# Kernel tuning notes

Hardware: AMD Instinct MI355X
Metric: run time of the kernel (lower is better)

The kernel has to match this reference:

```python
import jax, jax.numpy as jnp
from jax import lax
import numpy as np

C_IN, D_INNER, D_STATE, OUT_CH = 20, 32, 8, 20
DT_RANK = max(1, D_INNER // 8)
B, H, W = 4, 384, 384
EPS = 1e-5


def layernorm(x, g, b):
    m = jnp.mean(x, axis=-1, keepdims=True)
    v = jnp.mean((x - m) ** 2, axis=-1, keepdims=True)
    return (x - m) * lax.rsqrt(v + EPS) * g + b


def ss1d(x, xw, dw, db, A_log, Dp):
    # x: (Bb, L, Dd). Mamba selective scan: h_t = exp(dt*A)*h_{t-1} + dt*B_t*u_t; y_t = C_t.h_t + D*u_t
    Bb, L, Dd = x.shape
    N = A_log.shape[1]
    xdbl = x @ xw.T                                   # (Bb, L, dtr+2N)
    dt_lo, Bm, Cm = jnp.split(xdbl, [DT_RANK, DT_RANK + N], axis=-1)
    dt = jax.nn.softplus(dt_lo @ dw.T + db)           # (Bb, L, Dd)
    A = -jnp.exp(A_log)                               # (Dd, N)

    def step(h, inp):
        dt_t, B_t, C_t, u_t = inp                     # (Bb,Dd),(Bb,N),(Bb,N),(Bb,Dd)
        dA = jnp.exp(dt_t[:, :, None] * A)            # (Bb, Dd, N)
        h = dA * h + (dt_t * u_t)[:, :, None] * B_t[:, None, :]
        y = jnp.einsum('bdn,bn->bd', h, C_t)
        return h, y

    xs = (jnp.moveaxis(dt, 1, 0), jnp.moveaxis(Bm, 1, 0),
          jnp.moveaxis(Cm, 1, 0), jnp.moveaxis(x, 1, 0))
    h0 = jnp.zeros((Bb, Dd, N), dtype=x.dtype)
    _, ys = lax.scan(step, h0, xs)
    return jnp.moveaxis(ys, 0, 1) + x * Dp


def setup_inputs() -> dict:
    key = jax.random.key(0)
    ks = jax.random.split(key, 16)
    s = lambda k, shp, sc=0.05: jax.random.normal(k, shp, dtype=jnp.float32) * sc
    A_log1 = jnp.log(jnp.broadcast_to(jnp.arange(1, D_STATE + 1, dtype=jnp.float32), (D_INNER, D_STATE)))
    return {
        'x': jax.random.normal(ks[0], (B, C_IN, H, W), dtype=jnp.float32),
        'norm_g': jnp.ones((C_IN,), jnp.float32),
        'norm_b': jnp.zeros((C_IN,), jnp.float32),
        'inproj_w': s(ks[1], (D_INNER, C_IN), 0.15),
        'dw_w': s(ks[2], (3, 3, 1, D_INNER), 0.2),
        'dw_b': jnp.zeros((D_INNER,), jnp.float32),
        'ssm_xw': s(ks[3], (4, DT_RANK + 2 * D_STATE, D_INNER), 0.1),
        'ssm_dw': s(ks[4], (4, D_INNER, DT_RANK), 0.5),
        'ssm_db': s(ks[5], (4, D_INNER), 0.5) - 3.0,
        'ssm_Alog': jnp.broadcast_to(A_log1, (4, D_INNER, D_STATE)).copy(),
        'ssm_D': jnp.ones((4, D_INNER), jnp.float32),
        'merge_g': jnp.ones((4 * D_INNER,), jnp.float32),
        'merge_b': jnp.zeros((4 * D_INNER,), jnp.float32),
        'merge_w': s(ks[6], (D_INNER, 4 * D_INNER), 0.1),
        'out_w': s(ks[7], (OUT_CH, D_INNER), 0.15),
        'out_b': jnp.zeros((OUT_CH,), jnp.float32),
    }


def reference(x, norm_g, norm_b, inproj_w, dw_w, dw_b, ssm_xw, ssm_dw, ssm_db,
              ssm_Alog, ssm_D, merge_g, merge_b, merge_w, out_w, out_b):
    Bx, C, Hx, Wx = x.shape
    h = jnp.transpose(x, (0, 2, 3, 1))                      # (B,H,W,C)
    h = layernorm(h, norm_g, norm_b)
    h = jax.nn.silu(h @ inproj_w.T)                          # (B,H,W,Dd)
    h = lax.conv_general_dilated(h, dw_w, (1, 1), 'SAME',
                                 dimension_numbers=('NHWC', 'HWIO', 'NHWC'),
                                 feature_group_count=D_INNER) + dw_b
    h = jax.nn.silu(h)                                       # (B,H,W,Dd)

    p = lambda i: (ssm_xw[i], ssm_dw[i], ssm_db[i], ssm_Alog[i], ssm_D[i])

    x_h = h.reshape(Bx * Hx, Wx, D_INNER)
    y_h_fwd = ss1d(x_h, *p(0)).reshape(Bx, Hx, Wx, D_INNER)
    y_h_bwd = ss1d(x_h[:, ::-1], *p(1))[:, ::-1].reshape(Bx, Hx, Wx, D_INNER)

    x_v = jnp.transpose(h, (0, 2, 1, 3)).reshape(Bx * Wx, Hx, D_INNER)
    y_v_fwd = jnp.transpose(ss1d(x_v, *p(2)).reshape(Bx, Wx, Hx, D_INNER), (0, 2, 1, 3))
    y_v_bwd = jnp.transpose(ss1d(x_v[:, ::-1], *p(3))[:, ::-1].reshape(Bx, Wx, Hx, D_INNER), (0, 2, 1, 3))

    y = jnp.concatenate([y_h_fwd, y_h_bwd, y_v_fwd, y_v_bwd], axis=-1)  # (B,H,W,4*Dd)
    y = layernorm(y, merge_g, merge_b)
    y = y @ merge_w.T                                        # (B,H,W,Dd)
    y = y @ out_w.T + out_b                                  # (B,H,W,out_ch)
    return jnp.transpose(y, (0, 3, 1, 2))                    # (B,out_ch,H,W)
```

## Files before the change

kernel.cpp:

```cpp
#include <hip/hip_runtime.h>

typedef unsigned short u16;
typedef unsigned int   u32;
typedef unsigned long long u64;
typedef float f2 __attribute__((ext_vector_type(2)));

#define CIN  20
#define DIN  32
#define BB   4
#define HH   384
#define WW   384
#define HW   147456
#define BHW  589824
#define EPSF 1e-5f
#define GUARD  65536
#define UGUARD 131072

__device__ __forceinline__ float bflo(u32 u) {
    union { u32 v; float f; } x; x.v = u << 16; return x.f;
}
__device__ __forceinline__ float bfhi(u32 u) {
    union { u32 v; float f; } x; x.v = u & 0xffff0000u; return x.f;
}
__device__ __forceinline__ float bf2f(u16 h) {
    union { u32 v; float f; } x; x.v = ((u32)h) << 16; return x.f;
}
__device__ __forceinline__ u16 f2bf(float f) {
    union { float f; u32 u; } v; v.f = f;
    u32 u = v.u;
    return (u16)((u + 0x7FFFu + ((u >> 16) & 1u)) >> 16);
}
__device__ __forceinline__ float silu_f(float a) {
    return a / (1.f + __expf(-a));
}
__device__ __forceinline__ float softplus_f(float z) {
    return (z > 15.f) ? z : __logf(1.f + __expf(z));
}

__global__ void k_prep(const float* __restrict__ ow, const float* __restrict__ mw,
                       const float* __restrict__ mg, const float* __restrict__ mb,
                       const float* __restrict__ ob,
                       float* __restrict__ Wt, float* __restrict__ rsum,
                       float* __restrict__ c0)
{
    __shared__ float mdot[DIN];
    int t = threadIdx.x;
    if (t < DIN) {
        float s = 0.f;
        for (int k = 0; k < 128; ++k) s += mw[t*128 + k] * mb[k];
        mdot[t] = s;
    }
    {
        int k = t;
        for (int o = 0; o < CIN; ++o) {
            float s = 0.f;
            for (int d = 0; d < DIN; ++d) s += ow[o*DIN + d] * mw[d*128 + k];
            Wt[k*CIN + o] = s * mg[k];
        }
    }
    __syncthreads();
    if (t < CIN) {
        float rs = 0.f;
        for (int k = 0; k < 128; ++k) rs += Wt[k*CIN + t];
        rsum[t] = rs;
        float c = ob[t];
        for (int d = 0; d < DIN; ++d) c += ow[t*DIN + d] * mdot[d];
        c0[t] = c;
    }
}

#define TS   16
#define HT   18
#define CPAD 36
__global__ __launch_bounds__(256) void k_lnconv(
    const float* __restrict__ x, const float* __restrict__ ng,
    const float* __restrict__ nb, const float* __restrict__ ipw,
    const float* __restrict__ cw, const float* __restrict__ cb,
    u16* __restrict__ h2)
{
    __shared__ __align__(16) float hs[HT*HT*CPAD];
    __shared__ __align__(16) f2 wln_s[CIN*16];
    __shared__ float g_s[CIN], b_s[CIN];
    __shared__ __align__(16) f2 wc_s[9*16];
    __shared__ __align__(16) f2 bc2_s[16];

    int tid = threadIdx.x;
    for (int i = tid; i < CIN*16; i += 256) {
        int c = i >> 4, j2 = i & 15;
        wln_s[i] = f2{ ipw[(2*j2)*CIN + c], ipw[(2*j2+1)*CIN + c] };
    }
    if (tid < CIN) { g_s[tid] = ng[tid]; b_s[tid] = nb[tid]; }
    if (tid < 144) wc_s[tid] = f2{ cw[2*tid], cw[2*tid+1] };
    if (tid >= 144 && tid < 160) {
        int i = tid - 144;
        bc2_s[i] = f2{ cb[2*i], cb[2*i+1] };
    }
    __syncthreads();

    int bx = blockIdx.x;
    int b  = bx / 576, t6 = bx % 576;
    int ty0 = (t6 / 24)*TS, tx0 = (t6 % 24)*TS;

    auto do_pixel = [&](int j) {
        int hy = j / HT, hx = j % HT;
        int gy = ty0 + hy - 1, gx = tx0 + hx - 1;
        float* hp = &hs[(hy*HT + hx)*CPAD];
        if (gy >= 0 && gy < HH && gx >= 0 && gx < WW) {
            int rem = gy*WW + gx;
            float v[CIN];
            float m = 0.f;
            #pragma unroll
            for (int c = 0; c < CIN; ++c) { v[c] = x[(b*CIN + c)*HW + rem]; m += v[c]; }
            m *= (1.f/CIN);
            float var = 0.f;
            #pragma unroll
            for (int c = 0; c < CIN; ++c) { float d = v[c]-m; var += d*d; }
            var *= (1.f/CIN);
            float rstd = rsqrtf(var + EPSF);
            #pragma unroll
            for (int c = 0; c < CIN; ++c) v[c] = (v[c]-m)*rstd*g_s[c] + b_s[c];

            f2 o2[16];
            #pragma unroll
            for (int j2 = 0; j2 < 16; ++j2) o2[j2] = f2{0.f, 0.f};
            #pragma unroll
            for (int c = 0; c < CIN; ++c) {
                f2 vc = { v[c], v[c] };
                const float4* wr = (const float4*)&wln_s[c*16];
                #pragma unroll
                for (int jq = 0; jq < 8; ++jq) {
                    float4 wp = wr[jq];
                    o2[2*jq]   = __builtin_elementwise_fma(f2{wp.x, wp.y}, vc, o2[2*jq]);
                    o2[2*jq+1] = __builtin_elementwise_fma(f2{wp.z, wp.w}, vc, o2[2*jq+1]);
                }
            }
            #pragma unroll
            for (int q = 0; q < 8; ++q) {
                float a0 = silu_f(o2[2*q].x),   a1 = silu_f(o2[2*q].y);
                float a2 = silu_f(o2[2*q+1].x), a3 = silu_f(o2[2*q+1].y);
                *(float4*)&hp[4*q] = make_float4(a0, a1, a2, a3);
            }
        } else {
            #pragma unroll
            for (int q = 0; q < 8; ++q)
                *(float4*)&hp[4*q] = make_float4(0.f, 0.f, 0.f, 0.f);
        }
    };

    do_pixel(tid);
    __syncthreads();
    if (tid < HT*HT - 256) do_pixel(256 + tid);
    __syncthreads();

    int ty = tid >> 4, tx = tid & 15;
    int gy = ty0 + ty, gx = tx0 + tx;
    int p  = b*HW + gy*WW + gx;

    f2 acc2[16];
    #pragma unroll
    for (int i = 0; i < 16; ++i) acc2[i] = bc2_s[i];

    #pragma unroll
    for (int k = 0; k < 9; ++k) {
        int dy = k/3, dx = k%3;
        const float* np = &hs[((ty+dy)*HT + (tx+dx))*CPAD];
        const f2* wk = &wc_s[k*16];
        #pragma unroll
        for (int q = 0; q < 8; ++q) {
            float4 t4 = *(const float4*)&np[4*q];
            acc2[2*q]   = __builtin_elementwise_fma(wk[2*q],   f2{t4.x, t4.y}, acc2[2*q]);
            acc2[2*q+1] = __builtin_elementwise_fma(wk[2*q+1], f2{t4.z, t4.w}, acc2[2*q+1]);
        }
    }

    u32 pk[16];
    #pragma unroll
    for (int i = 0; i < 16; ++i) {
        float a = silu_f(acc2[i].x);
        float c = silu_f(acc2[i].y);
        pk[i] = (u32)f2bf(a) | ((u32)f2bf(c) << 16);
    }
    uint4* dst = (uint4*)(h2 + (size_t)p*DIN);
    dst[0] = make_uint4(pk[0],pk[1],pk[2],pk[3]);
    dst[1] = make_uint4(pk[4],pk[5],pk[6],pk[7]);
    dst[2] = make_uint4(pk[8],pk[9],pk[10],pk[11]);
    dst[3] = make_uint4(pk[12],pk[13],pk[14],pk[15]);
}

__global__ __launch_bounds__(256) void k_proj(
    const u16* __restrict__ h2, const float* __restrict__ xw,
    u16* __restrict__ dlA, u16* __restrict__ bcA)
{
    __shared__ __align__(16) f2 xw2_s[4*DIN*10];
    for (int i = threadIdx.x; i < 4*DIN*10; i += 256) {
        int dir = i / 320, r = i % 320;
        int d = r / 10, j2 = r % 10;
        xw2_s[i] = f2{ xw[(dir*CIN + 2*j2)*DIN + d],
                       xw[(dir*CIN + 2*j2 + 1)*DIN + d] };
    }
    __syncthreads();

    int p = (blockIdx.x*256 + threadIdx.x)*2;
    float ua[DIN], ub[DIN];
    const uint4* src = (const uint4*)(h2 + (size_t)p*DIN);
    #pragma unroll
    for (int q4 = 0; q4 < 4; ++q4) {
        uint4 v = src[q4];
        ua[q4*8+0]=bflo(v.x); ua[q4*8+1]=bfhi(v.x);
        ua[q4*8+2]=bflo(v.y); ua[q4*8+3]=bfhi(v.y);
        ua[q4*8+4]=bflo(v.z); ua[q4*8+5]=bfhi(v.z);
        ua[q4*8+6]=bflo(v.w); ua[q4*8+7]=bfhi(v.w);
        uint4 w = src[q4+4];
        ub[q4*8+0]=bflo(w.x); ub[q4*8+1]=bfhi(w.x);
        ub[q4*8+2]=bflo(w.y); ub[q4*8+3]=bfhi(w.y);
        ub[q4*8+4]=bflo(w.z); ub[q4*8+5]=bfhi(w.z);
        ub[q4*8+6]=bflo(w.w); ub[q4*8+7]=bfhi(w.w);
    }
    #pragma unroll 1
    for (int dir = 0; dir < 4; ++dir) {
        f2 xa[10], xb[10];
        #pragma unroll
        for (int j2 = 0; j2 < 10; ++j2) { xa[j2] = f2{0.f,0.f}; xb[j2] = f2{0.f,0.f}; }
        #pragma unroll
        for (int d = 0; d < DIN; ++d) {
            f2 uda = { ua[d], ua[d] };
            f2 udb = { ub[d], ub[d] };
            const float4* wr = (const float4*)&xw2_s[(dir*DIN + d)*10];
            #pragma unroll
            for (int jq = 0; jq < 5; ++jq) {
                float4 wp = wr[jq];
                f2 wlo = {wp.x, wp.y}, whi = {wp.z, wp.w};
                xa[2*jq]   = __builtin_elementwise_fma(wlo, uda, xa[2*jq]);
                xa[2*jq+1] = __builtin_elementwise_fma(whi, uda, xa[2*jq+1]);
                xb[2*jq]   = __builtin_elementwise_fma(wlo, udb, xb[2*jq]);
                xb[2*jq+1] = __builtin_elementwise_fma(whi, udb, xb[2*jq+1]);
            }
        }
        u32 pa[10], pb[10];
        #pragma unroll
        for (int i = 0; i < 10; ++i) {
            pa[i] = (u32)f2bf(xa[i].x) | ((u32)f2bf(xa[i].y) << 16);
            pb[i] = (u32)f2bf(xb[i].x) | ((u32)f2bf(xb[i].y) << 16);
        }
        *(uint4*)(dlA + (size_t)(dir*BHW + p)*4) = make_uint4(pa[0], pa[1], pb[0], pb[1]);
        uint4* bcd = (uint4*)(bcA + (size_t)(dir*BHW + p)*16);
        bcd[0] = make_uint4(pa[2], pa[3], pa[4], pa[5]);
        bcd[1] = make_uint4(pa[6], pa[7], pa[8], pa[9]);
        bcd[2] = make_uint4(pb[2], pb[3], pb[4], pb[5]);
        bcd[3] = make_uint4(pb[6], pb[7], pb[8], pb[9]);
    }
}

__global__ __launch_bounds__(256) void k_scan(
    const char* __restrict__ h2b,
    const char* __restrict__ dlb_,
    const char* __restrict__ bcb_,
    const float* __restrict__ Alog, const float* __restrict__ Dp,
    const float* __restrict__ dwm,  const float* __restrict__ dbv,
    char* __restrict__ y4b)
{
    int tid  = blockIdx.x*256 + threadIdx.x;
    int wv   = tid >> 6, lane = tid & 63;
    int half = lane >> 5, d = lane & 31;
    int dir  = wv / 768;
    int s    = (wv % 768)*2 + half;
    int b    = s / 384, r = s % 384;

    int p0, stp;
    if (dir == 0)      { p0 = b*HW + r*WW;           stp = 1;  }
    else if (dir == 1) { p0 = b*HW + r*WW + (WW-1);  stp = -1; }
    else if (dir == 2) { p0 = b*HW + r;              stp = WW; }
    else               { p0 = b*HW + (HH-1)*WW + r;  stp = -WW;}

    float Av[8];
    bool okl = true;
    #pragma unroll
    for (int j = 0; j < 8; ++j) {
        float e = __expf(Alog[(dir*DIN + d)*8 + j]);
        Av[j] = -e;
        okl = okl && (__builtin_fabsf(e - (float)(j+1)) < 2e-3f);
    }
    bool fast = (__ballot(okl) == ~0ull);

    float Dd  = Dp[dir*DIN + d];
    float dw0 = dwm[(dir*DIN + d)*4 + 0], dw1 = dwm[(dir*DIN + d)*4 + 1];
    float dw2 = dwm[(dir*DIN + d)*4 + 2], dw3 = dwm[(dir*DIN + d)*4 + 3];
    float dbc = dbv[dir*DIN + d];

    u32 uo = UGUARD + (u32)((p0*DIN + d)*2);           int su = stp*DIN*2;
    u32 yo = (u32)((dir*BHW + p0)*64 + d*2);           int sy = stp*64;
    u32 c1 = GUARD + (u32)((dir*BHW + p0)*8);          int s1 = stp*8;
    u32 c2 = GUARD + (u32)((dir*BHW + p0)*32);         int s2 = stp*32;

    u16 ub[4]; uint2 dlr[4]; uint4 B4[4], C4[4];
    u32 fu = uo, f1 = c1, f2o = c2;

    auto fetch = [&](int sl) {
        ub[sl]  = *(const u16*)(h2b + fu);
        dlr[sl] = *(const uint2*)(dlb_ + f1);
        B4[sl]  = *(const uint4*)(bcb_ + f2o);
        C4[sl]  = *(const uint4*)(bcb_ + f2o + 16);
        fu += (u32)su; f1 += (u32)s1; f2o += (u32)s2;
    };

    #pragma unroll
    for (int i = 0; i < 4; ++i) fetch(i);

    f2 h0 = {0.f,0.f}, h1v = {0.f,0.f}, h2v = {0.f,0.f}, h3 = {0.f,0.f};

    if (fast) {
        f2 a01, a23, a45, a67;
        f2 Bq0, Bq1, Bq2, Bq3;
        f2 Cp0, Cp1, Cp2, Cp3;
        float ydc;

        auto prep = [&](int sl) {
            float uu = bf2f(ub[sl]);
            uint2 dl = dlr[sl];
            uint4 Bv = B4[sl], Cv = C4[sl];
            float z = dbc + dw0*bflo(dl.x) + dw1*bfhi(dl.x)
                          + dw2*bflo(dl.y) + dw3*bfhi(dl.y);
            z = fminf(z, 80.f);
            float ez = __expf(z);
            float w  = 1.f + ez;
            float rr = __builtin_amdgcn_rcpf(w);
            float dt = __logf(w);
            float r2 = rr*rr;
            f2 rr2 = {r2, r2};
            f2 t01 = {rr, r2};
            a01 = t01;
            a23 = t01*rr2;
            a45 = a23*rr2;
            a67 = a45*rr2;
            float dtu = dt*uu;
            f2 du2 = {dtu, dtu};
            f2 Bp0 = { bflo(Bv.x), bfhi(Bv.x) }, Bp1 = { bflo(Bv.y), bfhi(Bv.y) };
            f2 Bp2 = { bflo(Bv.z), bfhi(Bv.z) }, Bp3 = { bflo(Bv.w), bfhi(Bv.w) };
            Bq0 = du2*Bp0; Bq1 = du2*Bp1; Bq2 = du2*Bp2; Bq3 = du2*Bp3;
            f2 c0 = { bflo(Cv.x), bfhi(Cv.x) }, c1v = { bflo(Cv.y), bfhi(Cv.y) };
            f2 c2v = { bflo(Cv.z), bfhi(Cv.z) }, c3 = { bflo(Cv.w), bfhi(Cv.w) };
            Cp0 = c0; Cp1 = c1v; Cp2 = c2v; Cp3 = c3;
            ydc = Dd*uu;
        };

        prep(0);

        #pragma unroll 4
        for (int t = 0; t < 384; ++t) {
            int sl = t & 3;
            fetch(sl);

            h0  = __builtin_elementwise_fma(a01, h0,  Bq0);
            h1v = __builtin_elementwise_fma(a23, h1v, Bq1);
            h2v = __builtin_elementwise_fma(a45, h2v, Bq2);
            h3  = __builtin_elementwise_fma(a67, h3,  Bq3);

            f2 yv = Cp0*h0;
            yv = __builtin_elementwise_fma(Cp1, h1v, yv);
            yv = __builtin_elementwise_fma(Cp2, h2v, yv);
            yv = __builtin_elementwise_fma(Cp3, h3,  yv);
            float y = yv.x + yv.y + ydc;

            prep((t+1) & 3);

            *(u16*)(y4b + yo) = f2bf(y);
            yo += (u32)sy;
        }
    } else {
        f2 A2[4];
        #pragma unroll
        for (int j = 0; j < 4; ++j) { A2[j].x = Av[2*j]; A2[j].y = Av[2*j+1]; }
        #pragma unroll 4
        for (int t = 0; t < 384; ++t) {
            int sl = t & 3;
            float uu = bf2f(ub[sl]);
            uint2 dl = dlr[sl];
            uint4 Bv = B4[sl], Cv = C4[sl];
            fetch(sl);

            float z = dbc + dw0*bflo(dl.x) + dw1*bfhi(dl.x)
                          + dw2*bflo(dl.y) + dw3*bfhi(dl.y);
            float dt = softplus_f(z);
            f2 dt2 = {dt, dt};
            f2 e0 = dt2*A2[0], e1 = dt2*A2[1], e2 = dt2*A2[2], e3 = dt2*A2[3];
            f2 a01 = { __expf(e0.x), __expf(e0.y) };
            f2 a23 = { __expf(e1.x), __expf(e1.y) };
            f2 a45 = { __expf(e2.x), __expf(e2.y) };
            f2 a67 = { __expf(e3.x), __expf(e3.y) };

            float dtu = dt*uu;
            f2 du2 = {dtu, dtu};
            f2 Bp0 = { bflo(Bv.x), bfhi(Bv.x) }, Bp1 = { bflo(Bv.y), bfhi(Bv.y) };
            f2 Bp2 = { bflo(Bv.z), bfhi(Bv.z) }, Bp3 = { bflo(Bv.w), bfhi(Bv.w) };
            f2 Cp0 = { bflo(Cv.x), bfhi(Cv.x) }, Cp1 = { bflo(Cv.y), bfhi(Cv.y) };
            f2 Cp2 = { bflo(Cv.z), bfhi(Cv.z) }, Cp3 = { bflo(Cv.w), bfhi(Cv.w) };

            h0  = __builtin_elementwise_fma(a01, h0,  du2*Bp0);
            h1v = __builtin_elementwise_fma(a23, h1v, du2*Bp1);
            h2v = __builtin_elementwise_fma(a45, h2v, du2*Bp2);
            h3  = __builtin_elementwise_fma(a67, h3,  du2*Bp3);

            f2 yv = Cp0*h0;
            yv = __builtin_elementwise_fma(Cp1, h1v, yv);
            yv = __builtin_elementwise_fma(Cp2, h2v, yv);
            yv = __builtin_elementwise_fma(Cp3, h3,  yv);

            float y = yv.x + yv.y + Dd*uu;
            *(u16*)(y4b + yo) = f2bf(y);
            yo += (u32)sy;
        }
    }
}

__global__ __launch_bounds__(256) void k_merge(
    const u16* __restrict__ y4, const float* __restrict__ Wt,
    const float* __restrict__ rsum, const float* __restrict__ c0,
    float* __restrict__ out)
{
    __shared__ __align__(16) f2 Wt2_s[128*10];
    __shared__ float rs_s[CIN], c0_s[CIN];
    for (int i = threadIdx.x; i < 128*10; i += 256) {
        int k = i / 10, o2 = i % 10;
        Wt2_s[i] = f2{ Wt[k*CIN + 2*o2], Wt[k*CIN + 2*o2 + 1] };
    }
    if (threadIdx.x < CIN) { rs_s[threadIdx.x] = rsum[threadIdx.x]; c0_s[threadIdx.x] = c0[threadIdx.x]; }
    __syncthreads();

    int p = (blockIdx.x*256 + threadIdx.x)*2;
    int b = p / HW, rem = p % HW;

    float s1a = 0.f, s2a = 0.f, s1b = 0.f, s2b = 0.f;
    f2 acca[10], accb[10];
    #pragma unroll
    for (int o2 = 0; o2 < 10; ++o2) { acca[o2] = f2{0.f,0.f}; accb[o2] = f2{0.f,0.f}; }

    #pragma unroll 1
    for (int dirk = 0; dirk < 4; ++dirk) {
        const uint4* src = (const uint4*)(y4 + ((size_t)dirk*BHW + p)*32);
        #pragma unroll
        for (int q4 = 0; q4 < 4; ++q4) {
            uint4 va = src[q4];
            uint4 vb = src[q4+4];
            u32 wa[4] = {va.x, va.y, va.z, va.w};
            u32 wb[4] = {vb.x, vb.y, vb.z, vb.w};
            #pragma unroll
            for (int i = 0; i < 4; ++i) {
                int k = dirk*32 + q4*8 + i*2;
                float aa = bflo(wa[i]); float ca = bfhi(wa[i]);
                float ab = bflo(wb[i]); float cb = bfhi(wb[i]);
                s1a += aa + ca; s2a += aa*aa + ca*ca;
                s1b += ab + cb; s2b += ab*ab + cb*cb;
                f2 afa = {aa, aa}, cfa = {ca, ca};
                f2 afb = {ab, ab}, cfb = {cb, cb};
                const float4* w0 = (const float4*)&Wt2_s[k*10];
                const float4* w1 = (const float4*)&Wt2_s[(k+1)*10];
                #pragma unroll
                for (int jq = 0; jq < 5; ++jq) {
                    float4 x0 = w0[jq], x1 = w1[jq];
                    f2 x0lo = {x0.x, x0.y}, x0hi = {x0.z, x0.w};
                    f2 x1lo = {x1.x, x1.y}, x1hi = {x1.z, x1.w};
                    acca[2*jq]   = __builtin_elementwise_fma(x0lo, afa, acca[2*jq]);
                    acca[2*jq]   = __builtin_elementwise_fma(x1lo, cfa, acca[2*jq]);
                    acca[2*jq+1] = __builtin_elementwise_fma(x0hi, afa, acca[2*jq+1]);
                    acca[2*jq+1] = __builtin_elementwise_fma(x1hi, cfa, acca[2*jq+1]);
                    accb[2*jq]   = __builtin_elementwise_fma(x0lo, afb, accb[2*jq]);
                    accb[2*jq]   = __builtin_elementwise_fma(x1lo, cfb, accb[2*jq]);
                    accb[2*jq+1] = __builtin_elementwise_fma(x0hi, afb, accb[2*jq+1]);
                    accb[2*jq+1] = __builtin_elementwise_fma(x1hi, cfb, accb[2*jq+1]);
                }
            }
        }
    }
    float ma = s1a*(1.f/128.f);
    float va = s2a*(1.f/128.f) - ma*ma;
    float ra = rsqrtf(va + EPSF);
    float mb2 = s1b*(1.f/128.f);
    float vb2 = s2b*(1.f/128.f) - mb2*mb2;
    float rb = rsqrtf(vb2 + EPSF);
    #pragma unroll
    for (int o2 = 0; o2 < 10; ++o2) {
        float a0 = ra*(acca[o2].x - ma*rs_s[2*o2])    + c0_s[2*o2];
        float a1 = ra*(acca[o2].y - ma*rs_s[2*o2+1])  + c0_s[2*o2+1];
        float b0 = rb*(accb[o2].x - mb2*rs_s[2*o2])   + c0_s[2*o2];
        float b1 = rb*(accb[o2].y - mb2*rs_s[2*o2+1]) + c0_s[2*o2+1];
        *(float2*)&out[(b*CIN + 2*o2)*HW + rem]   = float2{a0, b0};
        *(float2*)&out[(b*CIN + 2*o2+1)*HW + rem] = float2{a1, b1};
    }
}

extern "C" void kernel_launch(void* const* d_in, const int* in_sizes, int n_in,
                              void* d_out, int out_size, void* d_ws, size_t ws_size,
                              hipStream_t stream)
{
    const float* x    = (const float*)d_in[0];
    const float* ng   = (const float*)d_in[1];
    const float* nb   = (const float*)d_in[2];
    const float* ipw  = (const float*)d_in[3];
    const float* cw   = (const float*)d_in[4];
    const float* cb   = (const float*)d_in[5];
    const float* xw   = (const float*)d_in[6];
    const float* dwm  = (const float*)d_in[7];
    const float* dbv  = (const float*)d_in[8];
    const float* Alog = (const float*)d_in[9];
    const float* Dpv  = (const float*)d_in[10];
    const float* mg   = (const float*)d_in[11];
    const float* mb   = (const float*)d_in[12];
    const float* mw   = (const float*)d_in[13];
    const float* ow   = (const float*)d_in[14];
    const float* ob   = (const float*)d_in[15];
    float* out = (float*)d_out;

    const size_t y4_bytes = (size_t)4*BHW*DIN*2;
    const size_t dl_bytes = (size_t)4*BHW*8;
    const size_t bc_bytes = (size_t)4*BHW*32;
    const size_t wt_bytes = (size_t)(128*CIN + 64)*4;

    char* ws = (char*)d_ws;
    u16* y4 = (u16*)ws;

    size_t dl_pos = y4_bytes + GUARD;
    size_t bc_pos = dl_pos + dl_bytes + GUARD;
    size_t wt_pos = bc_pos + bc_bytes + GUARD;
    size_t need   = wt_pos + wt_bytes + GUARD;

    if (ws_size < need) {
        hipMemsetAsync(d_out, 0x7F, (size_t)out_size*4, stream);
        return;
    }

    char* h2base = (char*)d_out;
    u16*  h2 = (u16*)(h2base + UGUARD);

    u16* dlA = (u16*)(ws + dl_pos);
    u16* bcA = (u16*)(ws + bc_pos);
    float* Wt   = (float*)(ws + wt_pos);
    float* rsum = Wt + 128*CIN;
    float* c0   = rsum + 32;

    k_prep  <<<1, 128, 0, stream>>>(ow, mw, mg, mb, ob, Wt, rsum, c0);
    k_lnconv<<<2304, 256, 0, stream>>>(x, ng, nb, ipw, cw, cb, h2);
    k_proj  <<<BHW/512, 256, 0, stream>>>(h2, xw, dlA, bcA);
    k_scan  <<<768, 256, 0, stream>>>(
        h2base, (const char*)(ws + dl_pos - GUARD), (const char*)(ws + bc_pos - GUARD),
        Alog, Dpv, dwm, dbv, (char*)y4);
    k_merge <<<BHW/512, 256, 0, stream>>>(y4, Wt, rsum, c0, out);
}
```

Baseline: 479.8 us.

## Fuse prep, layernorm-conv and x-projection into a single front kernel

Merges k_prep, k_lnconv and k_proj into one kernel, k_front. Each thread now computes the per-direction x-projection (dt, B, C) straight from its in-register fp32 SiLU outputs instead of re-reading h2 from global memory as bf16. The projection weights reuse the conv tile's shared memory after a barrier, and block 0 also computes the merge-weight precompute. This removes two launches and one full pass over h2, at the cost of more register pressure and one extra shared-memory reload per block. The projection now uses unrounded fp32 activations, so its values can differ slightly.

```diff
diff --git a/kernel.cpp b/kernel.cpp
--- a/kernel.cpp
+++ b/kernel.cpp
@@ -37,52 +37,29 @@
     return (z > 15.f) ? z : __logf(1.f + __expf(z));
 }
 
-__global__ void k_prep(const float* __restrict__ ow, const float* __restrict__ mw,
-                       const float* __restrict__ mg, const float* __restrict__ mb,
-                       const float* __restrict__ ob,
-                       float* __restrict__ Wt, float* __restrict__ rsum,
-                       float* __restrict__ c0)
-{
-    __shared__ float mdot[DIN];
-    int t = threadIdx.x;
-    if (t < DIN) {
-        float s = 0.f;
-        for (int k = 0; k < 128; ++k) s += mw[t*128 + k] * mb[k];
-        mdot[t] = s;
-    }
-    {
-        int k = t;
-        for (int o = 0; o < CIN; ++o) {
-            float s = 0.f;
-            for (int d = 0; d < DIN; ++d) s += ow[o*DIN + d] * mw[d*128 + k];
-            Wt[k*CIN + o] = s * mg[k];
-        }
-    }
-    __syncthreads();
-    if (t < CIN) {
-        float rs = 0.f;
-        for (int k = 0; k < 128; ++k) rs += Wt[k*CIN + t];
-        rsum[t] = rs;
-        float c = ob[t];
-        for (int d = 0; d < DIN; ++d) c += ow[t*DIN + d] * mdot[d];
-        c0[t] = c;
-    }
-}
-
 #define TS   16
 #define HT   18
 #define CPAD 36
-__global__ __launch_bounds__(256) void k_lnconv(
+__global__ __launch_bounds__(256) void k_front(
     const float* __restrict__ x, const float* __restrict__ ng,
     const float* __restrict__ nb, const float* __restrict__ ipw,
     const float* __restrict__ cw, const float* __restrict__ cb,
-    u16* __restrict__ h2)
+    const float* __restrict__ xw,
+    const float* __restrict__ ow, const float* __restrict__ mw,
+    const float* __restrict__ mg, const float* __restrict__ mb,
+    const float* __restrict__ ob,
+    u16* __restrict__ h2, u16* __restrict__ dlA, u16* __restrict__ bcA,
+    float* __restrict__ Wt, float* __restrict__ rsum, float* __restrict__ c0)
 {
-    __shared__ __align__(16) float hs[HT*HT*CPAD];
+    __shared__ __align__(16) float sraw[HT*HT*CPAD];
     __shared__ __align__(16) f2 wln_s[CIN*16];
     __shared__ float g_s[CIN], b_s[CIN];
     __shared__ __align__(16) f2 wc_s[9*16];
     __shared__ __align__(16) f2 bc2_s[16];
+    __shared__ float mdot[DIN];
+
+    float* hs = sraw;
+    f2* xw2_s = (f2*)sraw;
 
     int tid = threadIdx.x;
     for (int i = tid; i < CIN*16; i += 256) {
@@ -173,26 +150,26 @@
         }
     }
 
-    u32 pk[16];
+    float u[DIN];
     #pragma unroll
     for (int i = 0; i < 16; ++i) {
-        float a = silu_f(acc2[i].x);
-        float c = silu_f(acc2[i].y);
-        pk[i] = (u32)f2bf(a) | ((u32)f2bf(c) << 16);
-    }
-    uint4* dst = (uint4*)(h2 + (size_t)p*DIN);
-    dst[0] = make_uint4(pk[0],pk[1],pk[2],pk[3]);
-    dst[1] = make_uint4(pk[4],pk[5],pk[6],pk[7]);
-    dst[2] = make_uint4(pk[8],pk[9],pk[10],pk[11]);
-    dst[3] = make_uint4(pk[12],pk[13],pk[14],pk[15]);
-}
-
-__global__ __launch_bounds__(256) void k_proj(
-    const u16* __restrict__ h2, const float* __restrict__ xw,
-    u16* __restrict__ dlA, u16* __restrict__ bcA)
-{
-    __shared__ __align__(16) f2 xw2_s[4*DIN*10];
-    for (int i = threadIdx.x; i < 4*DIN*10; i += 256) {
+        u[2*i]   = silu_f(acc2[i].x);
+        u[2*i+1] = silu_f(acc2[i].y);
+    }
+    {
+        u32 pk[16];
+        #pragma unroll
+        for (int i = 0; i < 16; ++i)
+            pk[i] = (u32)f2bf(u[2*i]) | ((u32)f2bf(u[2*i+1]) << 16);
+        uint4* dst = (uint4*)(h2 + (size_t)p*DIN);
+        dst[0] = make_uint4(pk[0],pk[1],pk[2],pk[3]);
+        dst[1] = make_uint4(pk[4],pk[5],pk[6],pk[7]);
+        dst[2] = make_uint4(pk[8],pk[9],pk[10],pk[11]);
+        dst[3] = make_uint4(pk[12],pk[13],pk[14],pk[15]);
+    }
+    __syncthreads();
+
+    for (int i = tid; i < 4*DIN*10; i += 256) {
         int dir = i / 320, r = i % 320;
         int d = r / 10, j2 = r % 10;
         xw2_s[i] = f2{ xw[(dir*CIN + 2*j2)*DIN + d],
@@ -200,54 +177,56 @@
     }
     __syncthreads();
 
-    int p = (blockIdx.x*256 + threadIdx.x)*2;
-    float ua[DIN], ub[DIN];
-    const uint4* src = (const uint4*)(h2 + (size_t)p*DIN);
-    #pragma unroll
-    for (int q4 = 0; q4 < 4; ++q4) {
-        uint4 v = src[q4];
-        ua[q4*8+0]=bflo(v.x); ua[q4*8+1]=bfhi(v.x);
-        ua[q4*8+2]=bflo(v.y); ua[q4*8+3]=bfhi(v.y);
-        ua[q4*8+4]=bflo(v.z); ua[q4*8+5]=bfhi(v.z);
-        ua[q4*8+6]=bflo(v.w); ua[q4*8+7]=bfhi(v.w);
-        uint4 w = src[q4+4];
-        ub[q4*8+0]=bflo(w.x); ub[q4*8+1]=bfhi(w.x);
-        ub[q4*8+2]=bflo(w.y); ub[q4*8+3]=bfhi(w.y);
-        ub[q4*8+4]=bflo(w.z); ub[q4*8+5]=bfhi(w.z);
-        ub[q4*8+6]=bflo(w.w); ub[q4*8+7]=bfhi(w.w);
-    }
     #pragma unroll 1
     for (int dir = 0; dir < 4; ++dir) {
-        f2 xa[10], xb[10];
-        #pragma unroll
-        for (int j2 = 0; j2 < 10; ++j2) { xa[j2] = f2{0.f,0.f}; xb[j2] = f2{0.f,0.f}; }
+        f2 xd2[10];
+        #pragma unroll
+        for (int j2 = 0; j2 < 10; ++j2) xd2[j2] = f2{0.f, 0.f};
         #pragma unroll
         for (int d = 0; d < DIN; ++d) {
-            f2 uda = { ua[d], ua[d] };
-            f2 udb = { ub[d], ub[d] };
+            f2 ud = { u[d], u[d] };
             const float4* wr = (const float4*)&xw2_s[(dir*DIN + d)*10];
             #pragma unroll
             for (int jq = 0; jq < 5; ++jq) {
                 float4 wp = wr[jq];
-                f2 wlo = {wp.x, wp.y}, whi = {wp.z, wp.w};
-                xa[2*jq]   = __builtin_elementwise_fma(wlo, uda, xa[2*jq]);
-                xa[2*jq+1] = __builtin_elementwise_fma(whi, uda, xa[2*jq+1]);
-                xb[2*jq]   = __builtin_elementwise_fma(wlo, udb, xb[2*jq]);
-                xb[2*jq+1] = __builtin_elementwise_fma(whi, udb, xb[2*jq+1]);
+                xd2[2*jq]   = __builtin_elementwise_fma(f2{wp.x, wp.y}, ud, xd2[2*jq]);
+                xd2[2*jq+1] = __builtin_elementwise_fma(f2{wp.z, wp.w}, ud, xd2[2*jq+1]);
             }
         }
-        u32 pa[10], pb[10];
-        #pragma unroll
-        for (int i = 0; i < 10; ++i) {
-            pa[i] = (u32)f2bf(xa[i].x) | ((u32)f2bf(xa[i].y) << 16);
-            pb[i] = (u32)f2bf(xb[i].x) | ((u32)f2bf(xb[i].y) << 16);
-        }
-        *(uint4*)(dlA + (size_t)(dir*BHW + p)*4) = make_uint4(pa[0], pa[1], pb[0], pb[1]);
+        u32 pk[10];
+        #pragma unroll
+        for (int i = 0; i < 10; ++i)
+            pk[i] = (u32)f2bf(xd2[i].x) | ((u32)f2bf(xd2[i].y) << 16);
+        *(uint2*)(dlA + (size_t)(dir*BHW + p)*4) = make_uint2(pk[0], pk[1]);
         uint4* bcd = (uint4*)(bcA + (size_t)(dir*BHW + p)*16);
-        bcd[0] = make_uint4(pa[2], pa[3], pa[4], pa[5]);
-        bcd[1] = make_uint4(pa[6], pa[7], pa[8], pa[9]);
-        bcd[2] = make_uint4(pb[2], pb[3], pb[4], pb[5]);
-        bcd[3] = make_uint4(pb[6], pb[7], pb[8], pb[9]);
+        bcd[0] = make_uint4(pk[2], pk[3], pk[4], pk[5]);
+        bcd[1] = make_uint4(pk[6], pk[7], pk[8], pk[9]);
+    }
+
+    if (bx == 0) {
+        int t = tid;
+        if (t < DIN) {
+            float s = 0.f;
+            for (int k = 0; k < 128; ++k) s += mw[t*128 + k] * mb[k];
+            mdot[t] = s;
+        }
+        if (t < 128) {
+            int k = t;
+            for (int o = 0; o < CIN; ++o) {
+                float s = 0.f;
+                for (int d = 0; d < DIN; ++d) s += ow[o*DIN + d] * mw[d*128 + k];
+                Wt[k*CIN + o] = s * mg[k];
+            }
+        }
+        __syncthreads();
+        if (t < CIN) {
+            float rs = 0.f;
+            for (int k = 0; k < 128; ++k) rs += Wt[k*CIN + t];
+            rsum[t] = rs;
+            float c = ob[t];
+            for (int d = 0; d < DIN; ++d) c += ow[t*DIN + d] * mdot[d];
+            c0[t] = c;
+        }
     }
 }
 
@@ -537,9 +516,9 @@
     float* rsum = Wt + 128*CIN;
     float* c0   = rsum + 32;
 
-    k_prep  <<<1, 128, 0, stream>>>(ow, mw, mg, mb, ob, Wt, rsum, c0);
-    k_lnconv<<<2304, 256, 0, stream>>>(x, ng, nb, ipw, cw, cb, h2);
-    k_proj  <<<BHW/512, 256, 0, stream>>>(h2, xw, dlA, bcA);
+    k_front <<<2304, 256, 0, stream>>>(x, ng, nb, ipw, cw, cb, xw,
+                                       ow, mw, mg, mb, ob,
+                                       h2, dlA, bcA, Wt, rsum, c0);
     k_scan  <<<768, 256, 0, stream>>>(
         h2base, (const char*)(ws + dl_pos - GUARD), (const char*)(ws + bc_pos - GUARD),
         Alog, Dpv, dwm, dbv, (char*)y4);
```

Result: no change. 471.0 us (-1.8%).
